# Kernel optimization log

Measured on AMD Instinct MI355X. Metric: run time of the kernel, lower is better.

## Reference

```python
import jax, jax.numpy as jnp
import numpy as np

F = 128   # flattened observation features
H = 64    # MLP/LSTM hidden size (hardcoded in module)
A = 15    # number of discrete actions
T = 128   # rollout length (timesteps)
B = 2048  # number of parallel envs (batch)


def setup_inputs() -> dict:
    key = jax.random.key(0)
    ks = jax.random.split(key, 12)
    n = lambda k, sh, s=1.0: jax.random.normal(k, sh, jnp.float32) * s
    return {
        "x": n(ks[0], (T * B, F)),
        "done": (jax.random.uniform(ks[1], (T * B,)) < 0.05).astype(jnp.float32),
        "h0": n(ks[2], (1, B, H)),
        "c0": n(ks[3], (1, B, H)),
        # MLP encoder params (Linear stores y = x @ W + b here, W: [in, out])
        "W1": n(ks[4], (F, H), 0.1), "b1": jnp.zeros((H,), jnp.float32),
        "W2": n(ks[5], (H, H), 0.1), "b2": jnp.zeros((H,), jnp.float32),
        # LSTM params, PyTorch layout: weight_ih [4H, H_in], gate order i,f,g,o
        "Wih": n(ks[6], (4 * H, H), 0.1), "bih": jnp.zeros((4 * H,), jnp.float32),
        "Whh": n(ks[7], (4 * H, H), 0.1), "bhh": jnp.zeros((4 * H,), jnp.float32),
        # actor / critic heads
        "Wa": n(ks[8], (H, A), 0.01), "ba": jnp.zeros((A,), jnp.float32),
        "Wc": n(ks[9], (H, 1), 1.0), "bc": jnp.zeros((1,), jnp.float32),
    }


def reference(x, done, h0, c0, W1, b1, W2, b2, Wih, bih, Whh, bhh, Wa, ba, Wc, bc):
    Bsz, Hh = h0.shape[1], h0.shape[2]
    # MLP encoder: Linear -> Tanh -> Linear -> Tanh
    y = jnp.tanh(x @ W1 + b1)
    y = jnp.tanh(y @ W2 + b2)                 # [T*B, H]
    y = y.reshape(-1, Bsz, Hh)                # [T, B, H]
    d = done.reshape(-1, Bsz)                 # [T, B]

    def step(carry, td):
        h, c = carry
        yt, dt = td
        m = (1.0 - dt)[:, None]               # done-mask hidden reset
        h = h * m
        c = c * m
        g = yt @ Wih.T + bih + h @ Whh.T + bhh  # [B, 4H]
        i, f, gg, o = jnp.split(g, 4, axis=-1)
        c = jax.nn.sigmoid(f) * c + jax.nn.sigmoid(i) * jnp.tanh(gg)
        h = jax.nn.sigmoid(o) * jnp.tanh(c)
        return (h, c), h

    (hT, cT), outs = jax.lax.scan(step, (h0[0], c0[0]), (y, d))
    z = outs.reshape(-1, Hh)                  # [T*B, H]
    logits = z @ Wa + ba                      # Categorical logits
    vf = z @ Wc + bc
    return logits, vf, hT[None], cT[None]
```

## Files before the change

### kernel.cpp

```cpp
#include <hip/hip_runtime.h>
#include <hip/hip_bf16.h>
#include <stdint.h>

typedef __bf16  bf16x8 __attribute__((ext_vector_type(8)));
typedef short   s16x8  __attribute__((ext_vector_type(8)));
typedef int     i32x4  __attribute__((ext_vector_type(4)));
typedef float   f32x4  __attribute__((ext_vector_type(4)));

union Frag { s16x8 s; bf16x8 b; i32x4 i; };

static __device__ __forceinline__ short f2bf(float f) {
    union { float f; unsigned u; } v; v.f = f;
    unsigned r = (v.u + 0x7FFFu + ((v.u >> 16) & 1u)) >> 16;
    return (short)r;
}
static __device__ __forceinline__ float bf2f(short s) {
    union { unsigned u; float f; } v; v.u = ((unsigned)(unsigned short)s) << 16;
    return v.f;
}
static __device__ __forceinline__ float fast_rcp(float x) { return __builtin_amdgcn_rcpf(x); }
static __device__ __forceinline__ float tanh_fast(float x) {
    float e = __expf(-2.0f * x);
    return (1.0f - e) * fast_rcp(1.0f + e);
}
static __device__ __forceinline__ f32x4 mfma16(bf16x8 a, bf16x8 b, f32x4 c) {
    return __builtin_amdgcn_mfma_f32_16x16x32_bf16(a, b, c, 0, 0, 0);
}

static __device__ __forceinline__ void block_sync_lds() {
    asm volatile("s_waitcnt lgkmcnt(0)\n\ts_barrier" ::: "memory");
}

#define GLDS(gp, lp) __builtin_amdgcn_global_load_lds( \
    (const __attribute__((address_space(1))) void*)(gp), \
    (__attribute__((address_space(3))) void*)(lp), 16, 0, 0)

#define TT 128
#define BB 2048
#define HH 64
#define FF 128
#define AA 15
#define CH 8
#define LOGITS_OFF 0
#define VF_OFF   3932160
#define HT_OFF   4194304
#define CT_OFF   4325376

static __device__ __forceinline__ void xload(
    const float* __restrict__ x, int t_x, int b0, int lane, int q, f32x4* xr)
{
    const float* xp = x + ((size_t)t_x*BB + b0 + (lane & 7))*FF + 8*q;
#pragma unroll
    for (int kf = 0; kf < 4; ++kf) {
        xr[2*kf]   = *(const f32x4*)(xp + 32*kf);
        xr[2*kf+1] = *(const f32x4*)(xp + 32*kf + 4);
    }
}
static __device__ __forceinline__ void mlp_l1(
    const f32x4* xr, const float* b1v, const short (*w1t)[136],
    int c, int q, f32x4* acc1)
{
    Frag af[4];
#pragma unroll
    for (int kf = 0; kf < 4; ++kf)
#pragma unroll
        for (int jj = 0; jj < 4; ++jj) {
            af[kf].s[jj]   = f2bf(xr[2*kf][jj]);
            af[kf].s[4+jj] = f2bf(xr[2*kf+1][jj]);
        }
#pragma unroll
    for (int ct = 0; ct < 4; ++ct) acc1[ct] = (f32x4){b1v[ct], b1v[ct], b1v[ct], b1v[ct]};
#pragma unroll
    for (int kf = 0; kf < 4; ++kf)
#pragma unroll
        for (int ct = 0; ct < 4; ++ct) {
            Frag bf; bf.s = *(const s16x8*)&w1t[16*ct + c][32*kf + 8*q];
            acc1[ct] = mfma16(af[kf].b, bf.b, acc1[ct]);
        }
}
static __device__ __forceinline__ void mlp_mid(
    const f32x4* acc1, short (*c1)[72], int c, int q, Frag* a2f)
{
    if (q < 2)
#pragma unroll
        for (int ct = 0; ct < 4; ++ct)
#pragma unroll
            for (int i = 0; i < 4; ++i)
                c1[4*q + i][16*ct + c] = f2bf(tanh_fast(acc1[ct][i]));
    a2f[0].s = *(const s16x8*)&c1[c & 7][8*q];
    a2f[1].s = *(const s16x8*)&c1[c & 7][32 + 8*q];
}
static __device__ __forceinline__ void mlp_l2(
    const Frag* a2f, const float* b2v, const short (*w2t)[72],
    short (*yout)[72], int c, int q)
{
    f32x4 acc2[4];
#pragma unroll
    for (int ct = 0; ct < 4; ++ct) acc2[ct] = (f32x4){b2v[ct], b2v[ct], b2v[ct], b2v[ct]};
#pragma unroll
    for (int kf = 0; kf < 2; ++kf)
#pragma unroll
        for (int ct = 0; ct < 4; ++ct) {
            Frag bf; bf.s = *(const s16x8*)&w2t[16*ct + c][32*kf + 8*q];
            acc2[ct] = mfma16(a2f[kf].b, bf.b, acc2[ct]);
        }
    if (q < 2)
#pragma unroll
        for (int ct = 0; ct < 4; ++ct)
#pragma unroll
            for (int i = 0; i < 4; ++i)
                yout[4*q + i][16*ct + c] = f2bf(tanh_fast(acc2[ct][i]));
}

__global__ __launch_bounds__(512, 1) void fused_kernel(
    const float* __restrict__ x, const float* __restrict__ done,
    const float* __restrict__ h0, const float* __restrict__ c0,
    const float* __restrict__ W1, const float* __restrict__ b1,
    const float* __restrict__ W2, const float* __restrict__ b2,
    const float* __restrict__ Wih, const float* __restrict__ bih,
    const float* __restrict__ Whh, const float* __restrict__ bhh,
    const float* __restrict__ Wa, const float* __restrict__ ba,
    const float* __restrict__ Wc, const float* __restrict__ bc,
    float* __restrict__ out_logits, float* __restrict__ out_vf,
    float* __restrict__ hT_out, float* __restrict__ cT_out)
{
    __shared__ short w1t[64][136];
    __shared__ short w2t[64][72];
    __shared__ short ybuf[2][CH][8][72];
    __shared__ short c1buf[4][8][72];
    __shared__ float obuf[2][CH][8][16];
    __shared__ short zbuf[2][8][72];
    __shared__ short hbuf[2][8][72];
    __shared__ float dbuf[TT+1][8];

    const int tid  = threadIdx.x;
    const int lane = tid & 63;
    const int w    = tid >> 6;
    const int c    = lane & 15;
    const int q    = lane >> 4;
    const int blk  = blockIdx.x;
    const int b0   = blk * 8;
    const bool crit = (w < 4);
    const int hw   = w - 4;
    const int r0   = 4*(q & 1) + 2*(q >> 1);

    Frag  wf[4][2];
    Frag  wfi[4][2];
    float biasv[4];
    Frag  hwf[2];
    float hbv = 0.f;
    float b1v[4] = {0,0,0,0}, b2v[4] = {0,0,0,0};
    float cst0 = 0.f, cst1 = 0.f;
    f32x4 gyr[4];
    f32x4 xr[8];
    f32x4 acc1[4];
    Frag  a2f[2];

    for (int i = tid; i < 128*64; i += 512) { int k = i >> 6, n = i & 63; w1t[n][k] = f2bf(W1[i]); }
    for (int i = tid; i < 64*64;  i += 512) { int k = i >> 6, n = i & 63; w2t[n][k] = f2bf(W2[i]); }

    if (crit) {
        const int jcol = 16*w + c;
#pragma unroll
        for (int a = 0; a < 4; ++a) {
            const int col = 64*a + jcol;
            biasv[a] = bih[col] + bhh[col];
#pragma unroll
            for (int kf = 0; kf < 2; ++kf) {
                const float* wp = Whh + (size_t)col*HH + 32*kf + 8*q;
                f32x4 w0 = *(const f32x4*)wp;
                f32x4 w1 = *(const f32x4*)(wp + 4);
#pragma unroll
                for (int jj = 0; jj < 4; ++jj) { wf[a][kf].s[jj] = f2bf(w0[jj]); wf[a][kf].s[4+jj] = f2bf(w1[jj]); }
                const float* vp = Wih + (size_t)col*HH + 32*kf + 8*q;
                f32x4 v0 = *(const f32x4*)vp;
                f32x4 v1 = *(const f32x4*)(vp + 4);
#pragma unroll
                for (int jj = 0; jj < 4; ++jj) { wfi[a][kf].s[jj] = f2bf(v0[jj]); wfi[a][kf].s[4+jj] = f2bf(v1[jj]); }
            }
        }
    } else {
        {
            const int t0 = hw * 32;
            const float* gp = done + (size_t)(t0 + (lane >> 1))*BB + b0 + 4*(lane & 1);
            GLDS(gp, &dbuf[t0][0]);
        }
#pragma unroll
        for (int kf = 0; kf < 2; ++kf)
#pragma unroll
            for (int jj = 0; jj < 8; ++jj) {
                int k = 32*kf + 8*q + jj;
                hwf[kf].s[jj] = f2bf((c < 15) ? Wa[k*AA + c] : Wc[k]);
            }
        hbv = (c < 15) ? ba[c] : bc[0];
#pragma unroll
        for (int ct = 0; ct < 4; ++ct) { b1v[ct] = b1[16*ct + c]; b2v[ct] = b2[16*ct + c]; }
        xload(x, 2*hw + 0, b0, lane, q, xr);
    }
    if (tid < 8) dbuf[TT][tid] = 0.0f;
    block_sync_lds();

    if (!crit) {
        mlp_l1(xr, b1v, w1t, c, q, acc1);
        mlp_mid(acc1, c1buf[hw], c, q, a2f);
        mlp_l2(a2f, b2v, w2t, ybuf[0][2*hw + 0], c, q);
        xload(x, 2*hw + 1, b0, lane, q, xr);
        mlp_l1(xr, b1v, w1t, c, q, acc1);
        mlp_mid(acc1, c1buf[hw], c, q, a2f);
        mlp_l2(a2f, b2v, w2t, ybuf[0][2*hw + 1], c, q);
        __builtin_amdgcn_s_waitcnt(0x0F70);
    }
    block_sync_lds();

    if (crit) {
        const int jcol = 16*w + c;
        {
            float d0 = dbuf[0][r0 + 0];
            float d1 = dbuf[0][r0 + 1];
            float cv0 = c0[(size_t)(b0 + r0 + 0)*HH + jcol];
            float cv1 = c0[(size_t)(b0 + r0 + 1)*HH + jcol];
            cst0 = (d0 != 0.0f) ? 0.0f : cv0;
            cst1 = (d1 != 0.0f) ? 0.0f : cv1;
        }
        if (tid < 128) {
            int mm = tid & 7, j4 = (tid >> 3) & 15;
            float dm = dbuf[0][mm];
            f32x4 hv = *(const f32x4*)(h0 + (size_t)(b0 + mm)*HH + 4*j4);
#pragma unroll
            for (int ii = 0; ii < 4; ++ii)
                hbuf[0][mm][4*j4 + ii] = (dm != 0.0f) ? (short)0 : f2bf(hv[ii]);
        }
        {
            Frag yc0, yc1;
            yc0.s = *(const s16x8*)&ybuf[0][0][lane & 7][8*q];
            yc1.s = *(const s16x8*)&ybuf[0][0][lane & 7][32 + 8*q];
#pragma unroll
            for (int a = 0; a < 4; ++a) {
                f32x4 g = (f32x4){biasv[a], biasv[a], biasv[a], biasv[a]};
                g = mfma16(yc0.b, wfi[a][0].b, g);
                g = mfma16(yc1.b, wfi[a][1].b, g);
                gyr[a] = g;
            }
        }
    }
    block_sync_lds();

    for (int tc = 0; tc < 16; ++tc) {
#pragma unroll
        for (int p = 0; p < 8; ++p) {
            const int t = 8*tc + p;
            if (crit) {
                const int jcol = 16*w + c;
                const int cur = p & 1;
                Frag hf0, hf1;
                hf0.s = *(const s16x8*)&hbuf[cur][lane & 7][8*q];
                hf1.s = *(const s16x8*)&hbuf[cur][lane & 7][32 + 8*q];
                f32x4 acc[4];
#pragma unroll
                for (int a = 0; a < 4; ++a) {
                    acc[a] = mfma16(hf0.b, wf[a][0].b, gyr[a]);
                    acc[a] = mfma16(hf1.b, wf[a][1].b, acc[a]);
                }
                const bool hiq = (q >= 2);
                float g0[4], g1[4];
#pragma unroll
                for (int a = 0; a < 4; ++a) {
                    g0[a] = hiq ? acc[a][2] : acc[a][0];
                    g1[a] = hiq ? acc[a][3] : acc[a][1];
                }
                const float dn0 = dbuf[t+1][r0 + 0];
                const float dn1 = dbuf[t+1][r0 + 1];
                if (tc < 15 || p < 7) {
                    const int ch = (p < 7) ? (tc & 1) : ((tc + 1) & 1);
                    const int sl = (p + 1) & 7;
                    Frag yc0, yc1;
                    yc0.s = *(const s16x8*)&ybuf[ch][sl][lane & 7][8*q];
                    yc1.s = *(const s16x8*)&ybuf[ch][sl][lane & 7][32 + 8*q];
#pragma unroll
                    for (int a = 0; a < 4; ++a) {
                        f32x4 g = (f32x4){biasv[a], biasv[a], biasv[a], biasv[a]};
                        g = mfma16(yc0.b, wfi[a][0].b, g);
                        g = mfma16(yc1.b, wfi[a][1].b, g);
                        gyr[a] = g;
                    }
                }
#define ELEM(GV, CSTV, RI, DN) {                                        \
                float ei = __expf(-GV[0]), ef = __expf(-GV[1]);         \
                float eg = __expf(-2.0f*GV[2]), eo = __expf(-GV[3]);    \
                float term = (1.0f - eg) * fast_rcp((1.0f + ei)*(1.0f + eg)); \
                float cn = fast_rcp(1.0f + ef)*CSTV + term;             \
                float ec = __expf(-2.0f*cn);                            \
                float hv = (1.0f - ec) * fast_rcp((1.0f + eo)*(1.0f + ec)); \
                short zb = f2bf(hv);                                    \
                zbuf[cur][RI][jcol] = zb;                               \
                const bool d = ((DN) != 0.0f);                          \
                CSTV = d ? 0.0f : cn;                                   \
                hbuf[cur ^ 1][RI][jcol] = d ? (short)0 : zb; }
                ELEM(g0, cst0, r0 + 0, dn0)
                ELEM(g1, cst1, r0 + 1, dn1)
#undef ELEM
            } else {
                if (p == 0 && tc < 15) xload(x, 8*(tc+1) + 2*hw + 0, b0, lane, q, xr);
                if (p == 1 && tc < 15) mlp_l1(xr, b1v, w1t, c, q, acc1);
                if (p == 2 && tc < 15) {
                    xload(x, 8*(tc+1) + 2*hw + 1, b0, lane, q, xr);
                    mlp_mid(acc1, c1buf[hw], c, q, a2f);
                }
                if (p == 3 && tc < 15) mlp_l2(a2f, b2v, w2t, ybuf[(tc+1) & 1][2*hw + 0], c, q);
                if (p == 4 && tc < 15) mlp_l1(xr, b1v, w1t, c, q, acc1);
                if (p == 5 && tc < 15) mlp_mid(acc1, c1buf[hw], c, q, a2f);
                if (p == 6 && tc < 15) mlp_l2(a2f, b2v, w2t, ybuf[(tc+1) & 1][2*hw + 1], c, q);
                if (p == 7 && tc >= 1 && w == 4) {
                    const int cc = tc - 1;
                    const int s = lane >> 3, r = lane & 7;
                    const size_t row = (size_t)(8*cc + s)*BB + b0 + r;
                    const float* ob = &obuf[cc & 1][s][r][0];
                    float* lp = out_logits + row*AA;
#pragma unroll
                    for (int n = 0; n < 15; ++n) lp[n] = ob[n];
                    out_vf[row] = ob[15];
                }
                if ((tc > 0 || p > 0) && w == 4 + (p & 3)) {
                    const int tp = t - 1;
                    Frag zf0, zf1;
                    zf0.s = *(const s16x8*)&zbuf[tp & 1][lane & 7][8*q];
                    zf1.s = *(const s16x8*)&zbuf[tp & 1][lane & 7][32 + 8*q];
                    f32x4 ha = (f32x4){hbv, hbv, hbv, hbv};
                    ha = mfma16(zf0.b, hwf[0].b, ha);
                    ha = mfma16(zf1.b, hwf[1].b, ha);
                    if (q < 2) {
#pragma unroll
                        for (int i = 0; i < 4; ++i)
                            obuf[(tp >> 3) & 1][tp & 7][4*q + i][c] = ha[i];
                    }
                }
            }
            block_sync_lds();
        }
    }

    if (!crit && w == 7) {
        Frag zf0, zf1;
        zf0.s = *(const s16x8*)&zbuf[1][lane & 7][8*q];
        zf1.s = *(const s16x8*)&zbuf[1][lane & 7][32 + 8*q];
        f32x4 ha = (f32x4){hbv, hbv, hbv, hbv};
        ha = mfma16(zf0.b, hwf[0].b, ha);
        ha = mfma16(zf1.b, hwf[1].b, ha);
        if (q < 2) {
#pragma unroll
            for (int i = 0; i < 4; ++i) obuf[1][7][4*q + i][c] = ha[i];
        }
    }
    __syncthreads();
    if (!crit && w == 4) {
        const int s = lane >> 3, r = lane & 7;
        const size_t row = (size_t)(120 + s)*BB + b0 + r;
        const float* ob = &obuf[1][s][r][0];
        float* lp = out_logits + row*AA;
#pragma unroll
        for (int n = 0; n < 15; ++n) lp[n] = ob[n];
        out_vf[row] = ob[15];
    }
    if (tid < 128) {
        int mm = tid & 7, j4 = (tid >> 3) & 15;
        f32x4 hv;
#pragma unroll
        for (int ii = 0; ii < 4; ++ii) hv[ii] = bf2f(zbuf[1][mm][4*j4 + ii]);
        *(f32x4*)(hT_out + (size_t)(b0 + mm)*HH + 4*j4) = hv;
    }
    if (crit) {
        const int jcol = 16*w + c;
        cT_out[(size_t)(b0 + r0 + 0)*HH + jcol] = cst0;
        cT_out[(size_t)(b0 + r0 + 1)*HH + jcol] = cst1;
    }
}

extern "C" void kernel_launch(void* const* d_in, const int* in_sizes, int n_in,
                              void* d_out, int out_size, void* d_ws, size_t ws_size,
                              hipStream_t stream) {
    const float* x    = (const float*)d_in[0];
    const float* done = (const float*)d_in[1];
    const float* h0   = (const float*)d_in[2];
    const float* c0   = (const float*)d_in[3];
    const float* W1   = (const float*)d_in[4];
    const float* b1   = (const float*)d_in[5];
    const float* W2   = (const float*)d_in[6];
    const float* b2   = (const float*)d_in[7];
    const float* Wih  = (const float*)d_in[8];
    const float* bih  = (const float*)d_in[9];
    const float* Whh  = (const float*)d_in[10];
    const float* bhh  = (const float*)d_in[11];
    const float* Wa   = (const float*)d_in[12];
    const float* ba   = (const float*)d_in[13];
    const float* Wc   = (const float*)d_in[14];
    const float* bc   = (const float*)d_in[15];
    float* out = (float*)d_out;

    (void)d_ws; (void)ws_size;

    fused_kernel<<<256, 512, 0, stream>>>(x, done, h0, c0, W1, b1, W2, b2,
                                          Wih, bih, Whh, bhh, Wa, ba, Wc, bc,
                                          out + LOGITS_OFF, out + VF_OFF,
                                          out + HT_OFF, out + CT_OFF);
}
```

Measured before the change: 297.8 us.

## Stage x tiles into double-buffered LDS via async global_load_lds prefetch

Replaces the register-based x loads with direct global-to-LDS async loads (global_load_lds) into a double-buffered, XOR-swizzled shared buffer, prefetching two chunks ahead. The MLP layer-1 then reads its fragments from LDS instead of holding 32 floats in registers. The goal is to hide global-load latency for x behind the recurrent LSTM phases and to free VGPRs. In exchange it adds roughly 64KB of LDS, extra waitcnt points and LDS read traffic.

```diff
diff --git a/kernel.cpp b/kernel.cpp
--- a/kernel.cpp
+++ b/kernel.cpp
@@ -46,28 +46,36 @@
 #define HT_OFF   4194304
 #define CT_OFF   4325376
 
-static __device__ __forceinline__ void xload(
-    const float* __restrict__ x, int t_x, int b0, int lane, int q, f32x4* xr)
+static __device__ __forceinline__ void stage_x(
+    const float* __restrict__ x, int t_x, int b0, int lane, float* dst)
 {
-    const float* xp = x + ((size_t)t_x*BB + b0 + (lane & 7))*FF + 8*q;
+    const int rh = lane >> 5;
+    const int k  = lane & 31;
+#pragma unroll
+    for (int j = 0; j < 4; ++j) {
+        const int row = 2*j + rh;
+        const float* gp = x + ((size_t)t_x*BB + b0 + row)*FF + ((k ^ row) << 2);
+        GLDS(gp, dst + j*256);
+    }
+}
+
+static __device__ __forceinline__ void mlp_l1(
+    const float* xt , const float* b1v,
+    const short (*w1t)[136], int lane, int c, int q, f32x4* acc1)
+{
+    const int row = lane & 7;
+    Frag af[4];
 #pragma unroll
     for (int kf = 0; kf < 4; ++kf) {
-        xr[2*kf]   = *(const f32x4*)(xp + 32*kf);
-        xr[2*kf+1] = *(const f32x4*)(xp + 32*kf + 4);
-    }
-}
-static __device__ __forceinline__ void mlp_l1(
-    const f32x4* xr, const float* b1v, const short (*w1t)[136],
-    int c, int q, f32x4* acc1)
-{
-    Frag af[4];
-#pragma unroll
-    for (int kf = 0; kf < 4; ++kf)
+        const int k0 = 8*kf + 2*q;
+        f32x4 x0 = *(const f32x4*)&xt[row*128 + (((k0    ) ^ row) << 2)];
+        f32x4 x1 = *(const f32x4*)&xt[row*128 + (((k0 + 1) ^ row) << 2)];
 #pragma unroll
         for (int jj = 0; jj < 4; ++jj) {
-            af[kf].s[jj]   = f2bf(xr[2*kf][jj]);
-            af[kf].s[4+jj] = f2bf(xr[2*kf+1][jj]);
-        }
+            af[kf].s[jj]   = f2bf(x0[jj]);
+            af[kf].s[4+jj] = f2bf(x1[jj]);
+        }
+    }
 #pragma unroll
     for (int ct = 0; ct < 4; ++ct) acc1[ct] = (f32x4){b1v[ct], b1v[ct], b1v[ct], b1v[ct]};
 #pragma unroll
@@ -124,6 +132,7 @@
     float* __restrict__ out_logits, float* __restrict__ out_vf,
     float* __restrict__ hT_out, float* __restrict__ cT_out)
 {
+    __shared__ float xbuf[2][CH][8][128];
     __shared__ short w1t[64][136];
     __shared__ short w2t[64][72];
     __shared__ short ybuf[2][CH][8][72];
@@ -152,7 +161,6 @@
     float b1v[4] = {0,0,0,0}, b2v[4] = {0,0,0,0};
     float cst0 = 0.f, cst1 = 0.f;
     f32x4 gyr[4];
-    f32x4 xr[8];
     f32x4 acc1[4];
     Frag  a2f[2];
 
@@ -186,6 +194,11 @@
             GLDS(gp, &dbuf[t0][0]);
         }
 #pragma unroll
+        for (int i = 0; i < 2; ++i) {
+            stage_x(x,     2*hw + i, b0, lane, &xbuf[0][2*hw + i][0][0]);
+            stage_x(x, 8 + 2*hw + i, b0, lane, &xbuf[1][2*hw + i][0][0]);
+        }
+#pragma unroll
         for (int kf = 0; kf < 2; ++kf)
 #pragma unroll
             for (int jj = 0; jj < 8; ++jj) {
@@ -195,20 +208,18 @@
         hbv = (c < 15) ? ba[c] : bc[0];
 #pragma unroll
         for (int ct = 0; ct < 4; ++ct) { b1v[ct] = b1[16*ct + c]; b2v[ct] = b2[16*ct + c]; }
-        xload(x, 2*hw + 0, b0, lane, q, xr);
     }
     if (tid < 8) dbuf[TT][tid] = 0.0f;
     block_sync_lds();
 
     if (!crit) {
-        mlp_l1(xr, b1v, w1t, c, q, acc1);
+        __builtin_amdgcn_s_waitcnt(0x0F70);
+        mlp_l1(&xbuf[0][2*hw + 0][0][0], b1v, w1t, lane, c, q, acc1);
         mlp_mid(acc1, c1buf[hw], c, q, a2f);
         mlp_l2(a2f, b2v, w2t, ybuf[0][2*hw + 0], c, q);
-        xload(x, 2*hw + 1, b0, lane, q, xr);
-        mlp_l1(xr, b1v, w1t, c, q, acc1);
+        mlp_l1(&xbuf[0][2*hw + 1][0][0], b1v, w1t, lane, c, q, acc1);
         mlp_mid(acc1, c1buf[hw], c, q, a2f);
         mlp_l2(a2f, b2v, w2t, ybuf[0][2*hw + 1], c, q);
-        __builtin_amdgcn_s_waitcnt(0x0F70);
     }
     block_sync_lds();
 
@@ -300,25 +311,30 @@
                 ELEM(g1, cst1, r0 + 1, dn1)
 #undef ELEM
             } else {
-                if (p == 0 && tc < 15) xload(x, 8*(tc+1) + 2*hw + 0, b0, lane, q, xr);
-                if (p == 1 && tc < 15) mlp_l1(xr, b1v, w1t, c, q, acc1);
-                if (p == 2 && tc < 15) {
-                    xload(x, 8*(tc+1) + 2*hw + 1, b0, lane, q, xr);
-                    mlp_mid(acc1, c1buf[hw], c, q, a2f);
-                }
+                if (p == 0 && tc <= 13) {
+#pragma unroll
+                    for (int i = 0; i < 2; ++i)
+                        stage_x(x, 8*(tc+2) + 2*hw + i, b0, lane,
+                                &xbuf[tc & 1][2*hw + i][0][0]);
+                }
+                if (p == 1 && tc < 15) mlp_l1(&xbuf[(tc+1) & 1][2*hw + 0][0][0], b1v, w1t, lane, c, q, acc1);
+                if (p == 2 && tc < 15) mlp_mid(acc1, c1buf[hw], c, q, a2f);
                 if (p == 3 && tc < 15) mlp_l2(a2f, b2v, w2t, ybuf[(tc+1) & 1][2*hw + 0], c, q);
-                if (p == 4 && tc < 15) mlp_l1(xr, b1v, w1t, c, q, acc1);
+                if (p == 4 && tc < 15) mlp_l1(&xbuf[(tc+1) & 1][2*hw + 1][0][0], b1v, w1t, lane, c, q, acc1);
                 if (p == 5 && tc < 15) mlp_mid(acc1, c1buf[hw], c, q, a2f);
                 if (p == 6 && tc < 15) mlp_l2(a2f, b2v, w2t, ybuf[(tc+1) & 1][2*hw + 1], c, q);
-                if (p == 7 && tc >= 1 && w == 4) {
-                    const int cc = tc - 1;
-                    const int s = lane >> 3, r = lane & 7;
-                    const size_t row = (size_t)(8*cc + s)*BB + b0 + r;
-                    const float* ob = &obuf[cc & 1][s][r][0];
-                    float* lp = out_logits + row*AA;
-#pragma unroll
-                    for (int n = 0; n < 15; ++n) lp[n] = ob[n];
-                    out_vf[row] = ob[15];
+                if (p == 7) {
+                    __builtin_amdgcn_s_waitcnt(0x0F70);
+                    if (tc >= 1 && w == 4) {
+                        const int cc = tc - 1;
+                        const int s = lane >> 3, r = lane & 7;
+                        const size_t row = (size_t)(8*cc + s)*BB + b0 + r;
+                        const float* ob = &obuf[cc & 1][s][r][0];
+                        float* lp = out_logits + row*AA;
+#pragma unroll
+                        for (int n = 0; n < 15; ++n) lp[n] = ob[n];
+                        out_vf[row] = ob[15];
+                    }
                 }
                 if ((tc > 0 || p > 0) && w == 4 + (p & 3)) {
                     const int tp = t - 1;
```

After: 285.8 us. -4.0%, faster.
